# Performance work log

Hardware: AMD Instinct MI355X
Metric: run time of the kernel (lower is better)

## Reference

```python
import jax, jax.numpy as jnp
import numpy as np

NUM_NODES = 100000
NUM_EDGES = 2500000
NUM_GRAPHS = 512
IN_DIM = 14
HID = 32
N_EXTRA_CONVS = 4  # num_layers - 1


def setup_inputs() -> dict:
    key = jax.random.key(0)
    ks = jax.random.split(key, 16)
    x = jax.random.normal(ks[0], (NUM_NODES, IN_DIM), dtype=jnp.float32)
    edge_index = jax.random.randint(ks[1], (2, NUM_EDGES), 0, NUM_NODES, dtype=jnp.int64)
    batch = jnp.sort(jax.random.randint(ks[2], (NUM_NODES,), 0, NUM_GRAPHS, dtype=jnp.int64))
    s = 1.0 / np.sqrt(HID)
    # PyG GraphConv: out = lin_rel(aggr_add(x_j)) + lin_root(x_i); lin_rel has bias, lin_root has no bias
    W_rel1 = jax.random.uniform(ks[3], (IN_DIM, HID), jnp.float32, -s, s)
    b_rel1 = jax.random.uniform(ks[4], (HID,), jnp.float32, -s, s)
    W_root1 = jax.random.uniform(ks[5], (IN_DIM, HID), jnp.float32, -s, s)
    W_rel = jax.random.uniform(ks[6], (N_EXTRA_CONVS, HID, HID), jnp.float32, -s, s)
    b_rel = jax.random.uniform(ks[7], (N_EXTRA_CONVS, HID), jnp.float32, -s, s)
    W_root = jax.random.uniform(ks[8], (N_EXTRA_CONVS, HID, HID), jnp.float32, -s, s)
    lin1_w = jax.random.uniform(ks[9], (HID, HID), jnp.float32, -s, s)
    lin1_b = jax.random.uniform(ks[10], (HID,), jnp.float32, -s, s)
    lin2_w = jax.random.uniform(ks[11], (HID, 2), jnp.float32, -s, s)
    lin2_b = jax.random.uniform(ks[12], (2,), jnp.float32, -s, s)
    return {
        "x": x, "W_rel1": W_rel1, "b_rel1": b_rel1, "W_root1": W_root1,
        "W_rel": W_rel, "b_rel": b_rel, "W_root": W_root,
        "lin1_w": lin1_w, "lin1_b": lin1_b, "lin2_w": lin2_w, "lin2_b": lin2_b,
        "edge_index": edge_index, "batch": batch,
    }


def reference(x, W_rel1, b_rel1, W_root1, W_rel, b_rel, W_root,
              lin1_w, lin1_b, lin2_w, lin2_b, edge_index, batch):
    src, dst = edge_index[0], edge_index[1]

    def graph_conv(h, wr, br, wroot):
        # sum-aggregate neighbor features: scatter-add messages h[src] into dst
        agg = jax.ops.segment_sum(h[src], dst, num_segments=NUM_NODES)
        return agg @ wr + br + h @ wroot

    h = jax.nn.relu(graph_conv(x, W_rel1, b_rel1, W_root1))
    for i in range(N_EXTRA_CONVS):
        h = jax.nn.relu(graph_conv(h, W_rel[i], b_rel[i], W_root[i]))
    # sum pooling per graph
    g = jax.ops.segment_sum(h, batch, num_segments=NUM_GRAPHS)
    g = jax.nn.relu(g @ lin1_w + lin1_b)
    # dropout is identity in eval mode
    logits = g @ lin2_w + lin2_b
    return jax.nn.log_softmax(logits, axis=1)
```

## Files before the change

kernel.cpp:

```cpp
#include <hip/hip_runtime.h>
#include <math.h>

#define N_NODES 100000
#define N_EDGES 2500000
#define N_GRAPHS 512
#define IN_DIM 14
#define HID 32
#define CAP 64

#define BSHIFT 7
#define BNODES 128
#define NB 782
#define NBP 784
#define NBANKS 8
#define SUBCAP 512
#define BCAP 4096
#define CHUNK 4096
#define TB_BIN 512
#define NBLK_E ((N_EDGES + CHUNK - 1) / CHUNK)
#define EPT (CHUNK / TB_BIN)

#define GSTRIDE 8
#define GCUR_N (NBP * NBANKS * GSTRIDE)

typedef unsigned int uint;
typedef unsigned short ushort;
typedef float v2f __attribute__((ext_vector_type(2)));

__device__ inline float bflo(uint w) { return __uint_as_float(w << 16); }
__device__ inline float bfhi(uint w) { return __uint_as_float(w & 0xffff0000u); }
__device__ inline ushort f2bf(float f) {
    uint u = __float_as_uint(f);
    return (ushort)((u + 0x7fffu + ((u >> 16) & 1u)) >> 16);
}

__global__ void bin_edges(const int* __restrict__ src, const int* __restrict__ dst,
                          int* __restrict__ gcur, int* __restrict__ binned) {
    __shared__ int scnt[NBP];
    __shared__ int sbase[NBP];
    int t = threadIdx.x;
    for (int i = t; i < NBP; i += TB_BIN) scnt[i] = 0;
    __syncthreads();
    int base = blockIdx.x * CHUNK;
    int bank = blockIdx.x & (NBANKS - 1);
    int dreg[EPT];
    int rreg[EPT];
#pragma unroll
    for (int j = 0; j < EPT; ++j) {
        int e = base + j * TB_BIN + t;
        dreg[j] = (e < N_EDGES) ? __builtin_nontemporal_load(dst + e) : -1;
        rreg[j] = (dreg[j] >= 0) ? atomicAdd(&scnt[dreg[j] >> BSHIFT], 1) : 0;
    }
    __syncthreads();
    for (int b = t; b < NBP; b += TB_BIN) {
        int c = scnt[b];
        sbase[b] = (c > 0) ? atomicAdd(&gcur[(bank * NBP + b) * GSTRIDE], c) : 0;
    }
    __syncthreads();
#pragma unroll
    for (int j = 0; j < EPT; ++j) {
        int d = dreg[j];
        if (d >= 0) {
            int e = base + j * TB_BIN + t;
            int b = d >> BSHIFT;
            int s = __builtin_nontemporal_load(src + e);
            int pos = sbase[b] + rreg[j];
            if (pos < SUBCAP)
                binned[b * BCAP + bank * SUBCAP + pos] = (s << BSHIFT) | (d & (BNODES - 1));
        }
    }
}

__global__ void build_slots(const int* __restrict__ gcur, const int* __restrict__ binned,
                            int* __restrict__ deg, int* __restrict__ slots) {
    __shared__ int stile[BNODES * CAP];
    __shared__ int sdeg[BNODES];
    int t = threadIdx.x;
    for (int i = t; i < BNODES * CAP; i += 256) stile[i] = N_NODES;
    if (t < BNODES) sdeg[t] = 0;
    __syncthreads();
    int b = blockIdx.x;
#pragma unroll
    for (int k = 0; k < NBANKS; ++k) {
        int cnt = gcur[(k * NBP + b) * GSTRIDE]; if (cnt > SUBCAP) cnt = SUBCAP;
        const int* seg = binned + b * BCAP + k * SUBCAP;
        for (int i = t; i < cnt; i += 256) {
            int w = __builtin_nontemporal_load(seg + i);
            int ld = w & (BNODES - 1), sn = w >> BSHIFT;
            int p = atomicAdd(&sdeg[ld], 1);
            if (p < CAP) stile[ld * CAP + p] = sn;
        }
    }
    __syncthreads();
    int nbase = b * BNODES;
    int rows = N_NODES - nbase; if (rows > BNODES) rows = BNODES;
    int r = t & 127, h = t >> 7;
    if (r < rows) {
        int dv = sdeg[r]; if (dv > CAP) dv = CAP;
        if (h == 0) deg[nbase + r] = dv;
        int n4 = ((dv + 15) >> 4) << 2;
        int4* drow = (int4*)(slots + (size_t)(nbase + r) * CAP);
        const int4* srow = (const int4*)(stile + r * CAP);
        for (int i = h; i < n4; i += 2) drow[i] = srow[i];
    }
}

__global__ void gemm14(const float* __restrict__ h, const float* __restrict__ W,
                       ushort* __restrict__ out, ushort* __restrict__ zrow2,
                       uint2* __restrict__ f0, uint2* __restrict__ f1) {
    __shared__ float sW[IN_DIM][HID];
    int t = threadIdx.x;
    for (int i = t; i < IN_DIM * HID; i += 256) sW[i / HID][i % HID] = W[i];
    if (blockIdx.x == 0) {
        if (t < 4) ((uint4*)(out + (size_t)N_NODES * HID))[t] = make_uint4(0, 0, 0, 0);
        else if (t < 8) ((uint4*)(zrow2 + (size_t)N_NODES * HID))[t - 4] = make_uint4(0, 0, 0, 0);
        else if (t < 12) f0[(size_t)N_NODES * 4 + (t - 8)] = make_uint2(0, 0);
        else if (t < 16) f1[(size_t)N_NODES * 4 + (t - 12)] = make_uint2(0, 0);
    }
    __syncthreads();
    int idx = blockIdx.x * 256 + t;
    if (idx >= N_NODES * HID) return;
    int n = idx >> 5, o = idx & 31;
    const float* hr = h + (long)n * IN_DIM;
    float acc = 0.f;
#pragma unroll
    for (int k = 0; k < IN_DIM; ++k) acc += hr[k] * sW[k][o];
    out[idx] = f2bf(acc);
}

template <bool MUL_REL, int K, bool ROOT_BF16, bool GBF8>
__global__ void conv_fused(const int* __restrict__ deg, const int* __restrict__ slots,
                           const void* __restrict__ gat,
                           const void* __restrict__ root_in,
                           const float* __restrict__ Wrel,
                           const float* __restrict__ bias,
                           const float* __restrict__ Wroot,
                           ushort* __restrict__ outb,
                           uint2* __restrict__ outf8) {
    __shared__ float sWrel[MUL_REL ? HID * HID : 1];
    __shared__ float sWroot[K * HID];
    __shared__ float sb[HID];
    int t = threadIdx.x;
    if (MUL_REL)
        for (int i = t; i < HID * HID; i += 256) sWrel[i] = Wrel[i];
    for (int i = t; i < K * HID; i += 256) sWroot[i] = Wroot[i];
    if (t < HID) sb[t] = bias[t];
    __syncthreads();

    int n = blockIdx.x * 64 + (t >> 2);
    if (n >= N_NODES) return;
    int q = t & 3;

    int dn = __builtin_nontemporal_load(deg + n); if (dn > CAP) dn = CAP;
    int rounds = (dn + 7) >> 3;
    const int* sl = slots + (size_t)n * CAP;
    int2 my[8];
#pragma unroll
    for (int r = 0; r < 8; ++r)
        if (r < rounds) {
            long w = __builtin_nontemporal_load((const long*)(sl + r * 8 + q * 2));
            my[r].x = (int)(w & 0xffffffffL);
            my[r].y = (int)(w >> 32);
        }

    float a[8] = {0.f, 0.f, 0.f, 0.f, 0.f, 0.f, 0.f, 0.f};
#pragma unroll
    for (int r = 0; r < 8; ++r) {
        if (r < rounds) {
#pragma unroll
            for (int j = 0; j < 8; ++j) {
                int c = __shfl((j & 1) ? my[r].y : my[r].x, j >> 1, 4);
                if constexpr (GBF8) {
                    uint2 v = ((const uint2*)gat)[(size_t)c * 4 + q];
                    v2f p0 = __builtin_amdgcn_cvt_pk_f32_bf8(v.x, false);
                    v2f p1 = __builtin_amdgcn_cvt_pk_f32_bf8(v.x, true);
                    v2f p2 = __builtin_amdgcn_cvt_pk_f32_bf8(v.y, false);
                    v2f p3 = __builtin_amdgcn_cvt_pk_f32_bf8(v.y, true);
                    a[0] += p0.x; a[1] += p0.y; a[2] += p1.x; a[3] += p1.y;
                    a[4] += p2.x; a[5] += p2.y; a[6] += p3.x; a[7] += p3.y;
                } else {
                    uint4 v = *(const uint4*)((const ushort*)gat + (size_t)c * HID + q * 8);
                    a[0] += bflo(v.x); a[1] += bfhi(v.x);
                    a[2] += bflo(v.y); a[3] += bfhi(v.y);
                    a[4] += bflo(v.z); a[5] += bfhi(v.z);
                    a[6] += bflo(v.w); a[7] += bfhi(v.w);
                }
            }
        }
    }

    float r8[8];
#pragma unroll
    for (int o = 0; o < 8; ++o) r8[o] = sb[q * 8 + o];

    if constexpr (MUL_REL) {
#pragma unroll
        for (int cl = 0; cl < 4; ++cl) {
#pragma unroll
            for (int j = 0; j < 8; ++j) {
                float av = __shfl(a[j], cl, 4);
                const float* w = &sWrel[(cl * 8 + j) * HID + q * 8];
#pragma unroll
                for (int o = 0; o < 8; ++o) r8[o] += av * w[o];
            }
        }
    } else {
#pragma unroll
        for (int o = 0; o < 8; ++o) r8[o] += a[o];
    }

    if constexpr (ROOT_BF16) {
        uint4 h4 = *(const uint4*)((const ushort*)root_in + (size_t)n * HID + q * 8);
        float hh[8] = {bflo(h4.x), bfhi(h4.x), bflo(h4.y), bfhi(h4.y),
                       bflo(h4.z), bfhi(h4.z), bflo(h4.w), bfhi(h4.w)};
#pragma unroll
        for (int cl = 0; cl < 4; ++cl) {
#pragma unroll
            for (int j = 0; j < 8; ++j) {
                float hv = __shfl(hh[j], cl, 4);
                const float* w = &sWroot[(cl * 8 + j) * HID + q * 8];
#pragma unroll
                for (int o = 0; o < 8; ++o) r8[o] += hv * w[o];
            }
        }
    } else {
        const float* hr = (const float*)root_in + (long)n * K;
#pragma unroll
        for (int k = 0; k < K; ++k) {
            float hv = hr[k];
            const float* w = &sWroot[k * HID + q * 8];
#pragma unroll
            for (int o = 0; o < 8; ++o) r8[o] += hv * w[o];
        }
    }

    float v[8];
#pragma unroll
    for (int o = 0; o < 8; ++o) v[o] = fmaxf(r8[o], 0.f);

    uint pw[4];
#pragma unroll
    for (int m = 0; m < 4; ++m)
        pw[m] = (uint)f2bf(v[2 * m]) | ((uint)f2bf(v[2 * m + 1]) << 16);
    *(uint4*)(outb + (size_t)n * HID + q * 8) = make_uint4(pw[0], pw[1], pw[2], pw[3]);

    uint w0 = __builtin_amdgcn_cvt_pk_bf8_f32(v[0], v[1], 0u, false);
    w0 = __builtin_amdgcn_cvt_pk_bf8_f32(v[2], v[3], w0, true);
    uint w1 = __builtin_amdgcn_cvt_pk_bf8_f32(v[4], v[5], 0u, false);
    w1 = __builtin_amdgcn_cvt_pk_bf8_f32(v[6], v[7], w1, true);
    outf8[(size_t)n * 4 + q] = make_uint2(w0, w1);
}

#define POOL_NODES 128
__global__ void pool_sum(const ushort* __restrict__ h, const int* __restrict__ batch,
                         float* __restrict__ g) {
    __shared__ int sbatch[POOL_NODES];
    int t = threadIdx.x;
    int nbase = blockIdx.x * POOL_NODES;
    for (int i = t; i < POOL_NODES; i += 256) {
        int n = nbase + i;
        sbatch[i] = (n < N_NODES) ? batch[n] : -1;
    }
    __syncthreads();
    int f = t & 31;
    int c0 = (t >> 5) * 16;
    int curb = -1;
    float acc = 0.f;
    for (int j = 0; j < 16; ++j) {
        int li = c0 + j;
        int n = nbase + li;
        if (n >= N_NODES) break;
        int bid = sbatch[li];
        float v = bflo((uint)h[(size_t)n * HID + f]);
        if (bid != curb) {
            if (curb >= 0) atomicAdd(&g[curb * HID + f], acc);
            curb = bid;
            acc = 0.f;
        }
        acc += v;
    }
    if (curb >= 0) atomicAdd(&g[curb * HID + f], acc);
}

__global__ void head(const float* __restrict__ g, const float* __restrict__ w1,
                     const float* __restrict__ b1, const float* __restrict__ w2,
                     const float* __restrict__ b2, float* __restrict__ out) {
    __shared__ float sW1[HID][HID];
    __shared__ float sW2[HID][2];
    __shared__ float sb1[HID];
    int t = threadIdx.x;
    for (int i = t; i < HID * HID; i += 128) sW1[i / HID][i % HID] = w1[i];
    if (t < HID * 2) sW2[t / 2][t % 2] = w2[t];
    if (t < HID) sb1[t] = b1[t];
    __syncthreads();
    int gid = blockIdx.x * 128 + t;
    float gi[HID];
#pragma unroll
    for (int k = 0; k < HID; ++k) gi[k] = g[gid * HID + k];
    float l0 = b2[0], l1 = b2[1];
#pragma unroll
    for (int o = 0; o < HID; ++o) {
        float a = sb1[o];
#pragma unroll
        for (int k = 0; k < HID; ++k) a += gi[k] * sW1[k][o];
        a = fmaxf(a, 0.f);
        l0 += a * sW2[o][0];
        l1 += a * sW2[o][1];
    }
    float m = fmaxf(l0, l1);
    float lse = m + logf(expf(l0 - m) + expf(l1 - m));
    out[gid * 2 + 0] = l0 - lse;
    out[gid * 2 + 1] = l1 - lse;
}

extern "C" void kernel_launch(void* const* d_in, const int* in_sizes, int n_in,
                              void* d_out, int out_size, void* d_ws, size_t ws_size,
                              hipStream_t stream) {
    const float* x      = (const float*)d_in[0];
    const float* W_rel1 = (const float*)d_in[1];
    const float* b_rel1 = (const float*)d_in[2];
    const float* W_root1= (const float*)d_in[3];
    const float* W_rel  = (const float*)d_in[4];
    const float* b_rel  = (const float*)d_in[5];
    const float* W_root = (const float*)d_in[6];
    const float* lin1_w = (const float*)d_in[7];
    const float* lin1_b = (const float*)d_in[8];
    const float* lin2_w = (const float*)d_in[9];
    const float* lin2_b = (const float*)d_in[10];
    const int*   ei     = (const int*)d_in[11];
    const int*   batch  = (const int*)d_in[12];
    float* out = (float*)d_out;

    const int* src = ei;
    const int* dst = ei + N_EDGES;

    int*    gcur   = (int*)d_ws;
    int*    binned = gcur + GCUR_N;
    int*    deg    = binned + NB * BCAP;
    int*    slots  = deg + N_NODES + 32;
    ushort* B0b    = (ushort*)(slots + (size_t)N_NODES * CAP);
    ushort* B1b    = B0b + (size_t)(N_NODES + 1) * HID;
    float*  g      = (float*)(B1b + (size_t)(N_NODES + 1) * HID);
    uint2*  F0     = (uint2*)(g + N_GRAPHS * HID);
    uint2*  F1     = F0 + (size_t)(N_NODES + 1) * 4;

    dim3 blk(256);
    dim3 grd_no((N_NODES * HID + 255) / 256);
    dim3 grd_cv((N_NODES + 63) / 64);
    dim3 grd_pl((N_NODES + POOL_NODES - 1) / POOL_NODES);

    hipMemsetAsync(gcur, 0, GCUR_N * sizeof(int), stream);
    bin_edges<<<dim3(NBLK_E), dim3(TB_BIN), 0, stream>>>(src, dst, gcur, binned);
    build_slots<<<dim3(NB), blk, 0, stream>>>(gcur, binned, deg, slots);

    gemm14<<<grd_no, blk, 0, stream>>>(x, W_rel1, B0b, B1b, F0, F1);
    conv_fused<false, IN_DIM, false, false><<<grd_cv, blk, 0, stream>>>(
        deg, slots, (const void*)B0b, (const void*)x, nullptr, b_rel1, W_root1, B1b, F1);

    ushort* cur = B1b;  uint2* curf = F1;
    ushort* nxt = B0b;  uint2* nxtf = F0;
    for (int i = 0; i < 4; ++i) {
        conv_fused<true, HID, true, true><<<grd_cv, blk, 0, stream>>>(
            deg, slots, (const void*)curf, (const void*)cur, W_rel + i * HID * HID,
            b_rel + i * HID, W_root + i * HID * HID, nxt, nxtf);
        ushort* ts = cur; cur = nxt; nxt = ts;
        uint2*  tf = curf; curf = nxtf; nxtf = tf;
    }

    hipMemsetAsync(g, 0, (size_t)N_GRAPHS * HID * sizeof(float), stream);
    pool_sum<<<grd_pl, blk, 0, stream>>>(cur, batch, g);
    head<<<dim3(4), dim3(128), 0, stream>>>(g, lin1_w, lin1_b, lin2_w, lin2_b, out);
}
```

Measured before the change: 341.2 us.

## Sort nodes by degree class so conv waves have uniform gather rounds

Adds three small kernels that bucket nodes by their number of 8-edge gather rounds and build a permutation plus permuted degree array. The five conv_fused launches then process nodes in this degree-sorted order, so lanes in a wavefront share similar loop trip counts and divergence drops. The cost is three extra launches and a memset, plus an indirection through nperm that scatters the root-feature and output row accesses instead of keeping them contiguous.

```diff
diff --git a/kernel.cpp b/kernel.cpp
--- a/kernel.cpp
+++ b/kernel.cpp
@@ -23,6 +23,10 @@
 #define GSTRIDE 8
 #define GCUR_N (NBP * NBANKS * GSTRIDE)
 
+#define NCLS 9
+#define CLS_BLK 1024
+#define NBLK_C ((N_NODES + CLS_BLK - 1) / CLS_BLK)
+
 typedef unsigned int uint;
 typedef unsigned short ushort;
 typedef float v2f __attribute__((ext_vector_type(2)));
@@ -105,6 +109,62 @@
     }
 }
 
+__global__ void cls_count(const int* __restrict__ deg, int* __restrict__ gtot) {
+    __shared__ int scnt[NCLS];
+    int t = threadIdx.x;
+    if (t < NCLS) scnt[t] = 0;
+    __syncthreads();
+    int base = blockIdx.x * CLS_BLK;
+    for (int i = t; i < CLS_BLK; i += 256) {
+        int n = base + i;
+        if (n < N_NODES) {
+            int dv = deg[n]; if (dv > CAP) dv = CAP;
+            atomicAdd(&scnt[(dv + 7) >> 3], 1);
+        }
+    }
+    __syncthreads();
+    if (t < NCLS && scnt[t] > 0) atomicAdd(&gtot[t], scnt[t]);
+}
+
+__global__ void cls_prefix(const int* __restrict__ gtot, int* __restrict__ gcls) {
+    if (threadIdx.x == 0) {
+        int s = 0;
+        for (int c = 0; c < NCLS; ++c) { gcls[c * GSTRIDE] = s; s += gtot[c]; }
+    }
+}
+
+__global__ void cls_scatter(const int* __restrict__ deg, int* __restrict__ gcls,
+                            int* __restrict__ nperm, int* __restrict__ degp) {
+    __shared__ int scnt[NCLS];
+    __shared__ int sbase[NCLS];
+    int t = threadIdx.x;
+    if (t < NCLS) scnt[t] = 0;
+    __syncthreads();
+    int base = blockIdx.x * CLS_BLK;
+    int dvreg[4], rcreg[4], rkreg[4];
+#pragma unroll
+    for (int j = 0; j < 4; ++j) {
+        int n = base + j * 256 + t;
+        if (n < N_NODES) {
+            int dv = deg[n]; if (dv > CAP) dv = CAP;
+            dvreg[j] = dv; rcreg[j] = (dv + 7) >> 3;
+            rkreg[j] = atomicAdd(&scnt[rcreg[j]], 1);
+        } else rcreg[j] = -1;
+    }
+    __syncthreads();
+    if (t < NCLS) sbase[t] = (scnt[t] > 0) ? atomicAdd(&gcls[t * GSTRIDE], scnt[t]) : 0;
+    __syncthreads();
+#pragma unroll
+    for (int j = 0; j < 4; ++j) {
+        if (rcreg[j] >= 0) {
+            int n = base + j * 256 + t;
+            int pos = sbase[rcreg[j]] + rkreg[j];
+            nperm[pos] = n;
+            degp[pos] = dvreg[j];
+        }
+    }
+}
+
 __global__ void gemm14(const float* __restrict__ h, const float* __restrict__ W,
                        ushort* __restrict__ out, ushort* __restrict__ zrow2,
                        uint2* __restrict__ f0, uint2* __restrict__ f1) {
@@ -129,7 +189,8 @@
 }
 
 template <bool MUL_REL, int K, bool ROOT_BF16, bool GBF8>
-__global__ void conv_fused(const int* __restrict__ deg, const int* __restrict__ slots,
+__global__ void conv_fused(const int* __restrict__ nperm, const int* __restrict__ degp,
+                           const int* __restrict__ slots,
                            const void* __restrict__ gat,
                            const void* __restrict__ root_in,
                            const float* __restrict__ Wrel,
@@ -147,11 +208,12 @@
     if (t < HID) sb[t] = bias[t];
     __syncthreads();
 
-    int n = blockIdx.x * 64 + (t >> 2);
-    if (n >= N_NODES) return;
+    int gid = blockIdx.x * 64 + (t >> 2);
+    if (gid >= N_NODES) return;
+    int n = nperm[gid];
     int q = t & 3;
 
-    int dn = __builtin_nontemporal_load(deg + n); if (dn > CAP) dn = CAP;
+    int dn = degp[gid];
     int rounds = (dn + 7) >> 3;
     const int* sl = slots + (size_t)n * CAP;
     int2 my[8];
@@ -343,6 +405,10 @@
     float*  g      = (float*)(B1b + (size_t)(N_NODES + 1) * HID);
     uint2*  F0     = (uint2*)(g + N_GRAPHS * HID);
     uint2*  F1     = F0 + (size_t)(N_NODES + 1) * 4;
+    int*    gtot   = (int*)(F1 + (size_t)(N_NODES + 1) * 4);
+    int*    gcls   = gtot + 16;
+    int*    nperm  = gcls + NCLS * GSTRIDE + 8;
+    int*    degp   = nperm + N_NODES + 32;
 
     dim3 blk(256);
     dim3 grd_no((N_NODES * HID + 255) / 256);
@@ -350,18 +416,23 @@
     dim3 grd_pl((N_NODES + POOL_NODES - 1) / POOL_NODES);
 
     hipMemsetAsync(gcur, 0, GCUR_N * sizeof(int), stream);
+    hipMemsetAsync(gtot, 0, 16 * sizeof(int), stream);
     bin_edges<<<dim3(NBLK_E), dim3(TB_BIN), 0, stream>>>(src, dst, gcur, binned);
     build_slots<<<dim3(NB), blk, 0, stream>>>(gcur, binned, deg, slots);
 
+    cls_count<<<dim3(NBLK_C), blk, 0, stream>>>(deg, gtot);
+    cls_prefix<<<dim3(1), dim3(64), 0, stream>>>(gtot, gcls);
+    cls_scatter<<<dim3(NBLK_C), blk, 0, stream>>>(deg, gcls, nperm, degp);
+
     gemm14<<<grd_no, blk, 0, stream>>>(x, W_rel1, B0b, B1b, F0, F1);
     conv_fused<false, IN_DIM, false, false><<<grd_cv, blk, 0, stream>>>(
-        deg, slots, (const void*)B0b, (const void*)x, nullptr, b_rel1, W_root1, B1b, F1);
+        nperm, degp, slots, (const void*)B0b, (const void*)x, nullptr, b_rel1, W_root1, B1b, F1);
 
     ushort* cur = B1b;  uint2* curf = F1;
     ushort* nxt = B0b;  uint2* nxtf = F0;
     for (int i = 0; i < 4; ++i) {
         conv_fused<true, HID, true, true><<<grd_cv, blk, 0, stream>>>(
-            deg, slots, (const void*)curf, (const void*)cur, W_rel + i * HID * HID,
+            nperm, degp, slots, (const void*)curf, (const void*)cur, W_rel + i * HID * HID,
             b_rel + i * HID, W_root + i * HID * HID, nxt, nxtf);
         ushort* ts = cur; cur = nxt; nxt = ts;
         uint2*  tf = curf; curf = nxtf; nxtf = tf;
```

After: 352.0 us. +3.2%, slower.

## Use two threads per node in conv_fused with wider gathers and packed accumulation

Applied to the files above, without the earlier changes.

Each node in the fused graph-conv kernel is now handled by 2 lanes instead of 4. Each lane gathers 16 features per neighbor with wider vector loads: uint4 for the bf8 path, two uint4 for the bf16 path. Accumulation uses packed float2 adds, and the grid is halved. This cuts shuffle and index overhead and raises bytes per load. In exchange each thread holds more registers and does twice the FMA work, and there is half as much thread-level parallelism for hiding gather latency.

```diff
diff --git a/kernel.cpp b/kernel.cpp
--- a/kernel.cpp
+++ b/kernel.cpp
@@ -32,6 +32,9 @@
 __device__ inline ushort f2bf(float f) {
     uint u = __float_as_uint(f);
     return (ushort)((u + 0x7fffu + ((u >> 16) & 1u)) >> 16);
+}
+__device__ inline int sel4(int4 v, int i) {
+    return i == 0 ? v.x : i == 1 ? v.y : i == 2 ? v.z : v.w;
 }
 
 __global__ void bin_edges(const int* __restrict__ src, const int* __restrict__ dst,
@@ -147,80 +150,95 @@
     if (t < HID) sb[t] = bias[t];
     __syncthreads();
 
-    int n = blockIdx.x * 64 + (t >> 2);
+    int n = blockIdx.x * 128 + (t >> 1);
     if (n >= N_NODES) return;
-    int q = t & 3;
-
-    int dn = __builtin_nontemporal_load(deg + n); if (dn > CAP) dn = CAP;
+    int q = t & 1;
+
+    int dn = deg[n]; if (dn > CAP) dn = CAP;
     int rounds = (dn + 7) >> 3;
     const int* sl = slots + (size_t)n * CAP;
-    int2 my[8];
+    int4 my[8];
 #pragma unroll
     for (int r = 0; r < 8; ++r)
-        if (r < rounds) {
-            long w = __builtin_nontemporal_load((const long*)(sl + r * 8 + q * 2));
-            my[r].x = (int)(w & 0xffffffffL);
-            my[r].y = (int)(w >> 32);
-        }
-
-    float a[8] = {0.f, 0.f, 0.f, 0.f, 0.f, 0.f, 0.f, 0.f};
+        if (r < rounds) my[r] = *(const int4*)(sl + r * 8 + q * 4);
+
+    v2f a2[8];
+#pragma unroll
+    for (int i = 0; i < 8; ++i) a2[i] = (v2f){0.f, 0.f};
+
 #pragma unroll
     for (int r = 0; r < 8; ++r) {
         if (r < rounds) {
 #pragma unroll
             for (int j = 0; j < 8; ++j) {
-                int c = __shfl((j & 1) ? my[r].y : my[r].x, j >> 1, 4);
+                int c = __shfl(sel4(my[r], j & 3), j >> 2, 2);
                 if constexpr (GBF8) {
-                    uint2 v = ((const uint2*)gat)[(size_t)c * 4 + q];
-                    v2f p0 = __builtin_amdgcn_cvt_pk_f32_bf8(v.x, false);
-                    v2f p1 = __builtin_amdgcn_cvt_pk_f32_bf8(v.x, true);
-                    v2f p2 = __builtin_amdgcn_cvt_pk_f32_bf8(v.y, false);
-                    v2f p3 = __builtin_amdgcn_cvt_pk_f32_bf8(v.y, true);
-                    a[0] += p0.x; a[1] += p0.y; a[2] += p1.x; a[3] += p1.y;
-                    a[4] += p2.x; a[5] += p2.y; a[6] += p3.x; a[7] += p3.y;
+                    uint4 v = ((const uint4*)gat)[(size_t)c * 2 + q];
+                    a2[0] += __builtin_amdgcn_cvt_pk_f32_bf8(v.x, false);
+                    a2[1] += __builtin_amdgcn_cvt_pk_f32_bf8(v.x, true);
+                    a2[2] += __builtin_amdgcn_cvt_pk_f32_bf8(v.y, false);
+                    a2[3] += __builtin_amdgcn_cvt_pk_f32_bf8(v.y, true);
+                    a2[4] += __builtin_amdgcn_cvt_pk_f32_bf8(v.z, false);
+                    a2[5] += __builtin_amdgcn_cvt_pk_f32_bf8(v.z, true);
+                    a2[6] += __builtin_amdgcn_cvt_pk_f32_bf8(v.w, false);
+                    a2[7] += __builtin_amdgcn_cvt_pk_f32_bf8(v.w, true);
                 } else {
-                    uint4 v = *(const uint4*)((const ushort*)gat + (size_t)c * HID + q * 8);
-                    a[0] += bflo(v.x); a[1] += bfhi(v.x);
-                    a[2] += bflo(v.y); a[3] += bfhi(v.y);
-                    a[4] += bflo(v.z); a[5] += bfhi(v.z);
-                    a[6] += bflo(v.w); a[7] += bfhi(v.w);
+                    const uint4* gp = (const uint4*)((const ushort*)gat + (size_t)c * HID + q * 16);
+                    uint4 v0 = gp[0];
+                    uint4 v1 = gp[1];
+                    a2[0] += (v2f){bflo(v0.x), bfhi(v0.x)};
+                    a2[1] += (v2f){bflo(v0.y), bfhi(v0.y)};
+                    a2[2] += (v2f){bflo(v0.z), bfhi(v0.z)};
+                    a2[3] += (v2f){bflo(v0.w), bfhi(v0.w)};
+                    a2[4] += (v2f){bflo(v1.x), bfhi(v1.x)};
+                    a2[5] += (v2f){bflo(v1.y), bfhi(v1.y)};
+                    a2[6] += (v2f){bflo(v1.z), bfhi(v1.z)};
+                    a2[7] += (v2f){bflo(v1.w), bfhi(v1.w)};
                 }
             }
         }
     }
 
-    float r8[8];
-#pragma unroll
-    for (int o = 0; o < 8; ++o) r8[o] = sb[q * 8 + o];
+    float a[16];
+#pragma unroll
+    for (int i = 0; i < 8; ++i) { a[2 * i] = a2[i].x; a[2 * i + 1] = a2[i].y; }
+
+    float r16[16];
+#pragma unroll
+    for (int o = 0; o < 16; ++o) r16[o] = sb[q * 16 + o];
 
     if constexpr (MUL_REL) {
 #pragma unroll
-        for (int cl = 0; cl < 4; ++cl) {
-#pragma unroll
-            for (int j = 0; j < 8; ++j) {
-                float av = __shfl(a[j], cl, 4);
-                const float* w = &sWrel[(cl * 8 + j) * HID + q * 8];
-#pragma unroll
-                for (int o = 0; o < 8; ++o) r8[o] += av * w[o];
+        for (int cl = 0; cl < 2; ++cl) {
+#pragma unroll
+            for (int j = 0; j < 16; ++j) {
+                float av = __shfl(a[j], cl, 2);
+                const float* w = &sWrel[(cl * 16 + j) * HID + q * 16];
+#pragma unroll
+                for (int o = 0; o < 16; ++o) r16[o] += av * w[o];
             }
         }
     } else {
 #pragma unroll
-        for (int o = 0; o < 8; ++o) r8[o] += a[o];
+        for (int o = 0; o < 16; ++o) r16[o] += a[o];
     }
 
     if constexpr (ROOT_BF16) {
-        uint4 h4 = *(const uint4*)((const ushort*)root_in + (size_t)n * HID + q * 8);
-        float hh[8] = {bflo(h4.x), bfhi(h4.x), bflo(h4.y), bfhi(h4.y),
-                       bflo(h4.z), bfhi(h4.z), bflo(h4.w), bfhi(h4.w)};
-#pragma unroll
-        for (int cl = 0; cl < 4; ++cl) {
-#pragma unroll
-            for (int j = 0; j < 8; ++j) {
-                float hv = __shfl(hh[j], cl, 4);
-                const float* w = &sWroot[(cl * 8 + j) * HID + q * 8];
-#pragma unroll
-                for (int o = 0; o < 8; ++o) r8[o] += hv * w[o];
+        const uint4* hp = (const uint4*)((const ushort*)root_in + (size_t)n * HID + q * 16);
+        uint4 h0 = hp[0];
+        uint4 h1 = hp[1];
+        float hh[16] = {bflo(h0.x), bfhi(h0.x), bflo(h0.y), bfhi(h0.y),
+                        bflo(h0.z), bfhi(h0.z), bflo(h0.w), bfhi(h0.w),
+                        bflo(h1.x), bfhi(h1.x), bflo(h1.y), bfhi(h1.y),
+                        bflo(h1.z), bfhi(h1.z), bflo(h1.w), bfhi(h1.w)};
+#pragma unroll
+        for (int cl = 0; cl < 2; ++cl) {
+#pragma unroll
+            for (int j = 0; j < 16; ++j) {
+                float hv = __shfl(hh[j], cl, 2);
+                const float* w = &sWroot[(cl * 16 + j) * HID + q * 16];
+#pragma unroll
+                for (int o = 0; o < 16; ++o) r16[o] += hv * w[o];
             }
         }
     } else {
@@ -228,27 +246,33 @@
 #pragma unroll
         for (int k = 0; k < K; ++k) {
             float hv = hr[k];
-            const float* w = &sWroot[k * HID + q * 8];
-#pragma unroll
-            for (int o = 0; o < 8; ++o) r8[o] += hv * w[o];
-        }
-    }
-
-    float v[8];
-#pragma unroll
-    for (int o = 0; o < 8; ++o) v[o] = fmaxf(r8[o], 0.f);
-
-    uint pw[4];
-#pragma unroll
-    for (int m = 0; m < 4; ++m)
+            const float* w = &sWroot[k * HID + q * 16];
+#pragma unroll
+            for (int o = 0; o < 16; ++o) r16[o] += hv * w[o];
+        }
+    }
+
+    float v[16];
+#pragma unroll
+    for (int o = 0; o < 16; ++o) v[o] = fmaxf(r16[o], 0.f);
+
+    uint pw[8];
+#pragma unroll
+    for (int m = 0; m < 8; ++m)
         pw[m] = (uint)f2bf(v[2 * m]) | ((uint)f2bf(v[2 * m + 1]) << 16);
-    *(uint4*)(outb + (size_t)n * HID + q * 8) = make_uint4(pw[0], pw[1], pw[2], pw[3]);
+    uint4* ob = (uint4*)(outb + (size_t)n * HID + q * 16);
+    ob[0] = make_uint4(pw[0], pw[1], pw[2], pw[3]);
+    ob[1] = make_uint4(pw[4], pw[5], pw[6], pw[7]);
 
     uint w0 = __builtin_amdgcn_cvt_pk_bf8_f32(v[0], v[1], 0u, false);
     w0 = __builtin_amdgcn_cvt_pk_bf8_f32(v[2], v[3], w0, true);
     uint w1 = __builtin_amdgcn_cvt_pk_bf8_f32(v[4], v[5], 0u, false);
     w1 = __builtin_amdgcn_cvt_pk_bf8_f32(v[6], v[7], w1, true);
-    outf8[(size_t)n * 4 + q] = make_uint2(w0, w1);
+    uint w2 = __builtin_amdgcn_cvt_pk_bf8_f32(v[8], v[9], 0u, false);
+    w2 = __builtin_amdgcn_cvt_pk_bf8_f32(v[10], v[11], w2, true);
+    uint w3 = __builtin_amdgcn_cvt_pk_bf8_f32(v[12], v[13], 0u, false);
+    w3 = __builtin_amdgcn_cvt_pk_bf8_f32(v[14], v[15], w3, true);
+    ((uint4*)(outf8 + (size_t)n * 4))[q] = make_uint4(w0, w1, w2, w3);
 }
 
 #define POOL_NODES 128
@@ -346,7 +370,7 @@
 
     dim3 blk(256);
     dim3 grd_no((N_NODES * HID + 255) / 256);
-    dim3 grd_cv((N_NODES + 63) / 64);
+    dim3 grd_cv((N_NODES + 127) / 128);
     dim3 grd_pl((N_NODES + POOL_NODES - 1) / POOL_NODES);
 
     hipMemsetAsync(gcur, 0, GCUR_N * sizeof(int), stream);
```

Measured after the change: 447.7 us. +31.2%, slower.

## Fuse graph sum-pooling and MLP head into one per-graph kernel

Applied to the files above, without the earlier changes.

Replaces the memset, the atomic-based pooling kernel and the separate head kernel with one kernel that launches a block per graph. Each block binary-searches the sorted batch array for its node range, reduces the node features in shared memory and then runs the two linear layers and log-softmax. This removes two launches, the memset and the global atomics. In exchange each block does serial binary searches, and work per block is uneven when graph sizes differ.

```diff
diff --git a/kernel.cpp b/kernel.cpp
--- a/kernel.cpp
+++ b/kernel.cpp
@@ -251,66 +251,61 @@
     outf8[(size_t)n * 4 + q] = make_uint2(w0, w1);
 }
 
-#define POOL_NODES 128
-__global__ void pool_sum(const ushort* __restrict__ h, const int* __restrict__ batch,
-                         float* __restrict__ g) {
-    __shared__ int sbatch[POOL_NODES];
-    int t = threadIdx.x;
-    int nbase = blockIdx.x * POOL_NODES;
-    for (int i = t; i < POOL_NODES; i += 256) {
-        int n = nbase + i;
-        sbatch[i] = (n < N_NODES) ? batch[n] : -1;
-    }
-    __syncthreads();
-    int f = t & 31;
-    int c0 = (t >> 5) * 16;
-    int curb = -1;
+__global__ __launch_bounds__(256) void pool_head(
+        const ushort* __restrict__ h, const int* __restrict__ batch,
+        const float* __restrict__ w1, const float* __restrict__ b1,
+        const float* __restrict__ w2, const float* __restrict__ b2,
+        float* __restrict__ out) {
+    __shared__ float sW1[HID][HID];
+    __shared__ float sb1[HID];
+    __shared__ float sW2[HID][2];
+    __shared__ float sacc[8][HID];
+    __shared__ float sg[HID];
+    __shared__ float sl[2][HID];
+    int t = threadIdx.x;
+    int gid = blockIdx.x;
+    for (int i = t; i < HID * HID; i += 256) sW1[i / HID][i % HID] = w1[i];
+    if (t < HID) sb1[t] = b1[t];
+    if (t < HID * 2) sW2[t >> 1][t & 1] = w2[t];
+
+    int lo = 0, hi = N_NODES;
+    while (lo < hi) { int m = (lo + hi) >> 1; if (batch[m] < gid) lo = m + 1; else hi = m; }
+    int s = lo;
+    hi = N_NODES;
+    while (lo < hi) { int m = (lo + hi) >> 1; if (batch[m] < gid + 1) lo = m + 1; else hi = m; }
+    int e = lo;
+
+    int f = t & 31, r = t >> 5;
     float acc = 0.f;
-    for (int j = 0; j < 16; ++j) {
-        int li = c0 + j;
-        int n = nbase + li;
-        if (n >= N_NODES) break;
-        int bid = sbatch[li];
-        float v = bflo((uint)h[(size_t)n * HID + f]);
-        if (bid != curb) {
-            if (curb >= 0) atomicAdd(&g[curb * HID + f], acc);
-            curb = bid;
-            acc = 0.f;
-        }
-        acc += v;
-    }
-    if (curb >= 0) atomicAdd(&g[curb * HID + f], acc);
-}
-
-__global__ void head(const float* __restrict__ g, const float* __restrict__ w1,
-                     const float* __restrict__ b1, const float* __restrict__ w2,
-                     const float* __restrict__ b2, float* __restrict__ out) {
-    __shared__ float sW1[HID][HID];
-    __shared__ float sW2[HID][2];
-    __shared__ float sb1[HID];
-    int t = threadIdx.x;
-    for (int i = t; i < HID * HID; i += 128) sW1[i / HID][i % HID] = w1[i];
-    if (t < HID * 2) sW2[t / 2][t % 2] = w2[t];
-    if (t < HID) sb1[t] = b1[t];
-    __syncthreads();
-    int gid = blockIdx.x * 128 + t;
-    float gi[HID];
-#pragma unroll
-    for (int k = 0; k < HID; ++k) gi[k] = g[gid * HID + k];
-    float l0 = b2[0], l1 = b2[1];
-#pragma unroll
-    for (int o = 0; o < HID; ++o) {
-        float a = sb1[o];
-#pragma unroll
-        for (int k = 0; k < HID; ++k) a += gi[k] * sW1[k][o];
+    for (int n = s + r; n < e; n += 8)
+        acc += bflo((uint)h[(size_t)n * HID + f]);
+    sacc[r][f] = acc;
+    __syncthreads();
+    if (t < HID) {
+        float gv = 0.f;
+#pragma unroll
+        for (int rr = 0; rr < 8; ++rr) gv += sacc[rr][t];
+        sg[t] = gv;
+    }
+    __syncthreads();
+    if (t < HID) {
+        float a = sb1[t];
+#pragma unroll
+        for (int k = 0; k < HID; ++k) a += sg[k] * sW1[k][t];
         a = fmaxf(a, 0.f);
-        l0 += a * sW2[o][0];
-        l1 += a * sW2[o][1];
-    }
-    float m = fmaxf(l0, l1);
-    float lse = m + logf(expf(l0 - m) + expf(l1 - m));
-    out[gid * 2 + 0] = l0 - lse;
-    out[gid * 2 + 1] = l1 - lse;
+        sl[0][t] = a * sW2[t][0];
+        sl[1][t] = a * sW2[t][1];
+    }
+    __syncthreads();
+    if (t == 0) {
+        float l0 = b2[0], l1 = b2[1];
+#pragma unroll
+        for (int o = 0; o < HID; ++o) { l0 += sl[0][o]; l1 += sl[1][o]; }
+        float m = fmaxf(l0, l1);
+        float lse = m + logf(expf(l0 - m) + expf(l1 - m));
+        out[gid * 2 + 0] = l0 - lse;
+        out[gid * 2 + 1] = l1 - lse;
+    }
 }
 
 extern "C" void kernel_launch(void* const* d_in, const int* in_sizes, int n_in,
@@ -340,14 +335,12 @@
     int*    slots  = deg + N_NODES + 32;
     ushort* B0b    = (ushort*)(slots + (size_t)N_NODES * CAP);
     ushort* B1b    = B0b + (size_t)(N_NODES + 1) * HID;
-    float*  g      = (float*)(B1b + (size_t)(N_NODES + 1) * HID);
-    uint2*  F0     = (uint2*)(g + N_GRAPHS * HID);
+    uint2*  F0     = (uint2*)(B1b + (size_t)(N_NODES + 1) * HID);
     uint2*  F1     = F0 + (size_t)(N_NODES + 1) * 4;
 
     dim3 blk(256);
     dim3 grd_no((N_NODES * HID + 255) / 256);
     dim3 grd_cv((N_NODES + 63) / 64);
-    dim3 grd_pl((N_NODES + POOL_NODES - 1) / POOL_NODES);
 
     hipMemsetAsync(gcur, 0, GCUR_N * sizeof(int), stream);
     bin_edges<<<dim3(NBLK_E), dim3(TB_BIN), 0, stream>>>(src, dst, gcur, binned);
@@ -367,7 +360,6 @@
         uint2*  tf = curf; curf = nxtf; nxtf = tf;
     }
 
-    hipMemsetAsync(g, 0, (size_t)N_GRAPHS * HID * sizeof(float), stream);
-    pool_sum<<<grd_pl, blk, 0, stream>>>(cur, batch, g);
-    head<<<dim3(4), dim3(128), 0, stream>>>(g, lin1_w, lin1_b, lin2_w, lin2_b, out);
-}
+    pool_head<<<dim3(N_GRAPHS), blk, 0, stream>>>(cur, batch, lin1_w, lin1_b,
+                                                  lin2_w, lin2_b, out);
+}
```

Measured after the change: 324.5 us. 1.05x faster.
